# Kernel tuning notes

Measured on AMD Instinct MI355X. Metric: run time of the kernel, lower is better.

Reference implementation:

```python
import jax, jax.numpy as jnp
import numpy as np
import math

B, N, C, H = 8, 1024, 768, 12
D = C // H
HID = 4 * C
LS_INIT = 1e-6
LN_EPS = 1e-5


def setup_inputs() -> dict:
    key = jax.random.key(0)
    ks = jax.random.split(key, 8)
    s = lambda fan: 1.0 / math.sqrt(fan)
    return {
        'x': jax.random.normal(ks[0], (B, N, C), jnp.float32),
        'ln1_w': jnp.ones((C,), jnp.float32),
        'ln1_b': jnp.zeros((C,), jnp.float32),
        'qkv_w': jax.random.uniform(ks[1], (3 * C, C), jnp.float32, -s(C), s(C)),
        'qkv_b': jnp.zeros((3 * C,), jnp.float32),
        'proj_w': jax.random.uniform(ks[2], (C, C), jnp.float32, -s(C), s(C)),
        'proj_b': jnp.zeros((C,), jnp.float32),
        'attn_bias': jnp.asarray(-math.log(N), jnp.float32),
        'ls1': jnp.full((C,), LS_INIT, jnp.float32),
        'ln2_w': jnp.ones((C,), jnp.float32),
        'ln2_b': jnp.zeros((C,), jnp.float32),
        'w1': jax.random.uniform(ks[3], (HID, C), jnp.float32, -s(C), s(C)),
        'b1': jnp.zeros((HID,), jnp.float32),
        'w2': jax.random.uniform(ks[4], (C, HID), jnp.float32, -s(HID), s(HID)),
        'b2': jnp.zeros((C,), jnp.float32),
        'ls2': jnp.full((C,), LS_INIT, jnp.float32),
    }


def _layernorm(x, w, b):
    mu = jnp.mean(x, axis=-1, keepdims=True)
    var = jnp.mean(jnp.square(x - mu), axis=-1, keepdims=True)
    return (x - mu) * jax.lax.rsqrt(var + LN_EPS) * w + b


def reference(x, ln1_w, ln1_b, qkv_w, qkv_b, proj_w, proj_b, attn_bias,
              ls1, ln2_w, ln2_b, w1, b1, w2, b2, ls2):
    # --- sigmoid attention branch ---
    h = _layernorm(x, ln1_w, ln1_b)                       # [B,N,C]
    qkv = h @ qkv_w.T + qkv_b                              # [B,N,3C]
    qkv = qkv.reshape(B, N, 3, H, D).transpose(2, 0, 3, 1, 4)
    q, k, v = qkv[0], qkv[1], qkv[2]                       # [B,H,N,D]
    scale = D ** -0.5
    scores = jnp.einsum('bhnd,bhmd->bhnm', q, k) * scale + attn_bias
    attn = jax.nn.sigmoid(scores)                          # [B,H,N,N]
    o = jnp.einsum('bhnm,bhmd->bhnd', attn, v)             # [B,H,N,D]
    o = o.transpose(0, 2, 1, 3).reshape(B, N, C)
    o = o @ proj_w.T + proj_b
    x = x + o * ls1
    # --- MLP branch ---
    h2 = _layernorm(x, ln2_w, ln2_b)
    m = jax.nn.gelu(h2 @ w1.T + b1, approximate=False)
    m = m @ w2.T + b2
    x = x + m * ls2
    return x
```

## Files before the change

### kernel.cpp

```cpp
#include <hip/hip_runtime.h>
#include <math.h>

static constexpr int Bv   = 8;
static constexpr int Nv   = 1024;
static constexpr int Cv   = 768;
static constexpr int Hv   = 12;
static constexpr int HIDv = 3072;
static constexpr int Mv   = Bv * Nv;

typedef __attribute__((ext_vector_type(4)))  float f32x4;
typedef __attribute__((ext_vector_type(16))) float f32x16;
typedef __attribute__((ext_vector_type(8)))  short s16x8;
typedef __attribute__((ext_vector_type(4)))  short s16x4;

__device__ __forceinline__ short f2bf(float f) {
  union { float f; unsigned u; } c; c.f = f;
  unsigned r = c.u + 0x7fffu + ((c.u >> 16) & 1u);
  return (short)(r >> 16);
}

__device__ __forceinline__ void gload16(const void* g, void* l) {
  __builtin_amdgcn_global_load_lds(
      (const __attribute__((address_space(1))) unsigned*)g,
      (__attribute__((address_space(3))) unsigned*)l, 16, 0, 0);
}

__device__ __forceinline__ unsigned ldsaddr(const void* p) {
  return (unsigned)(size_t)(const __attribute__((address_space(3))) char*)p;
}

__device__ __forceinline__ float fsigmoid_exp2(float t) {
  return __builtin_amdgcn_rcpf(1.0f + __builtin_amdgcn_exp2f(t));
}

__global__ __launch_bounds__(256) void cvt4_kernel(const float* __restrict__ w0,
                                                   const float* __restrict__ w1,
                                                   const float* __restrict__ w2,
                                                   const float* __restrict__ w3,
                                                   short* __restrict__ o0,
                                                   short* __restrict__ o1,
                                                   short* __restrict__ o2,
                                                   short* __restrict__ o3) {
  int bid = blockIdx.x;
  const float* in; short* out; int i;
  if (bid < 1728)      { in = w0; out = o0; i = bid * 256 + threadIdx.x; }
  else if (bid < 2304) { in = w1; out = o1; i = (bid - 1728) * 256 + threadIdx.x; }
  else if (bid < 4608) { in = w2; out = o2; i = (bid - 2304) * 256 + threadIdx.x; }
  else                 { in = w3; out = o3; i = (bid - 4608) * 256 + threadIdx.x; }
  float4 v = ((const float4*)in)[i];
  short4 o;
  o.x = f2bf(v.x); o.y = f2bf(v.y); o.z = f2bf(v.z); o.w = f2bf(v.w);
  ((short4*)out)[i] = o;
}

__global__ __launch_bounds__(256) void ln_kernel(const float* __restrict__ x,
                                                 const float* __restrict__ w,
                                                 const float* __restrict__ b,
                                                 short* __restrict__ out) {
  const int wv = threadIdx.x >> 6, l = threadIdx.x & 63;
  const int row = blockIdx.x * 4 + wv;
  const float4* xr = (const float4*)(x + (size_t)row * Cv);
  float4 v[3];
  float s = 0.f, s2 = 0.f;
#pragma unroll
  for (int c = 0; c < 3; ++c) {
    v[c] = xr[c * 64 + l];
    s  += v[c].x + v[c].y + v[c].z + v[c].w;
    s2 += v[c].x * v[c].x + v[c].y * v[c].y + v[c].z * v[c].z + v[c].w * v[c].w;
  }
#pragma unroll
  for (int o = 32; o; o >>= 1) { s += __shfl_xor(s, o); s2 += __shfl_xor(s2, o); }
  const float mu  = s * (1.f / Cv);
  const float var = s2 * (1.f / Cv) - mu * mu;
  const float rs  = rsqrtf(var + 1e-5f);
  short4* orow = (short4*)(out + (size_t)row * Cv);
  const float4* wp = (const float4*)w;
  const float4* bp = (const float4*)b;
#pragma unroll
  for (int c = 0; c < 3; ++c) {
    float4 wv4 = wp[c * 64 + l], bv4 = bp[c * 64 + l];
    short4 o4;
    o4.x = f2bf((v[c].x - mu) * rs * wv4.x + bv4.x);
    o4.y = f2bf((v[c].y - mu) * rs * wv4.y + bv4.y);
    o4.z = f2bf((v[c].z - mu) * rs * wv4.z + bv4.z);
    o4.w = f2bf((v[c].w - mu) * rs * wv4.w + bv4.w);
    orow[c * 64 + l] = o4;
  }
}

template <int EPI>
__global__ __launch_bounds__(256) void gemm_bt(const short* __restrict__ A,
                                               const short* __restrict__ Bw,
                                               int Nn, int K,
                                               const float* __restrict__ bias,
                                               short* __restrict__ outB) {
  __shared__ __align__(16) short ldsA[2][128 * 32];
  __shared__ __align__(16) short ldsB[2][128 * 32];
  const int tid = threadIdx.x, w = tid >> 6, l = tid & 63;
  const int nbx = Nn >> 7;
  const int cpx = (int)gridDim.x >> 3;
  const int wg = ((int)blockIdx.x & 7) * cpx + ((int)blockIdx.x >> 3);
  const int bx = wg % nbx, by = wg / nbx;
  const int rowBase = by << 7, colBase = bx << 7;
  const int nK = K >> 5;
  const int wr = w >> 1, wc = w & 1;
  const int lrow = l >> 2, lcb = (l & 3) * 8;

  f32x4 acc[4][4] = {};

  auto stage = [&](int buf, int kt) {
    const short* abase = A  + (size_t)rowBase * K + kt * 32;
    const short* bbase = Bw + (size_t)colBase * K + kt * 32;
#pragma unroll
    for (int i = 0; i < 2; ++i) {
      int r = w * 2 + i;
      gload16(abase + (size_t)(r * 16 + lrow) * K + lcb, &ldsA[buf][r * 512]);
      gload16(bbase + (size_t)(r * 16 + lrow) * K + lcb, &ldsB[buf][r * 512]);
    }
  };

  stage(0, 0);
  __syncthreads();
  int cur = 0;
  for (int kt = 0; kt < nK; ++kt) {
    if (kt + 1 < nK) stage(cur ^ 1, kt + 1);
    s16x8 af[4], bfr[4];
#pragma unroll
    for (int i = 0; i < 4; ++i) {
      af[i]  = *(const s16x8*)&ldsA[cur][(wr * 64 + i * 16 + (l & 15)) * 32 + (l >> 4) * 8];
      bfr[i] = *(const s16x8*)&ldsB[cur][(wc * 64 + i * 16 + (l & 15)) * 32 + (l >> 4) * 8];
    }
#pragma unroll
    for (int i = 0; i < 4; ++i)
#pragma unroll
      for (int j = 0; j < 4; ++j)
        acc[i][j] = __builtin_amdgcn_mfma_f32_16x16x32_bf16(af[i], bfr[j], acc[i][j], 0, 0, 0);
    __syncthreads();
    cur ^= 1;
  }

#pragma unroll
  for (int i = 0; i < 4; ++i)
#pragma unroll
    for (int j = 0; j < 4; ++j) {
      const int col = colBase + wc * 64 + j * 16 + (l & 15);
      const float bcol = bias[col];
#pragma unroll
      for (int r4 = 0; r4 < 4; ++r4) {
        const int row = rowBase + wr * 64 + i * 16 + (l >> 4) * 4 + r4;
        float v = acc[i][j][r4] + bcol;
        if (EPI == 2) v = v * fsigmoid_exp2(v * -2.4554669f);
        outB[(size_t)row * Nn + col] = f2bf(v);
      }
    }
}

template <int EPI>
__global__ __launch_bounds__(256) void gemm_sm(const short* __restrict__ A,
                                               const short* __restrict__ Bw,
                                               int Nn, int K,
                                               const float* __restrict__ bias,
                                               const float* __restrict__ ls,
                                               const float* __restrict__ resid,
                                               float* __restrict__ outF) {
  __shared__ __align__(16) short ldsA[2][64 * 32];
  __shared__ __align__(16) short ldsB[2][128 * 32];
  const int tid = threadIdx.x, w = tid >> 6, l = tid & 63;
  const int nbx = Nn >> 7;
  const int cpx = (int)gridDim.x >> 3;
  const int wg = ((int)blockIdx.x & 7) * cpx + ((int)blockIdx.x >> 3);
  const int bx = wg % nbx, by = wg / nbx;
  const int rowBase = by << 6, colBase = bx << 7;
  const int nK = K >> 5;
  const int wr = w >> 1, wc = w & 1;
  const int lrow = l >> 2, lcb = (l & 3) * 8;

  f32x4 acc[2][4] = {};

  auto stage = [&](int buf, int kt) {
    const short* abase = A  + (size_t)rowBase * K + kt * 32;
    const short* bbase = Bw + (size_t)colBase * K + kt * 32;
    gload16(abase + (size_t)(w * 16 + lrow) * K + lcb, &ldsA[buf][w * 512]);
#pragma unroll
    for (int i = 0; i < 2; ++i) {
      int r = w * 2 + i;
      gload16(bbase + (size_t)(r * 16 + lrow) * K + lcb, &ldsB[buf][r * 512]);
    }
  };

  stage(0, 0);
  __syncthreads();
  int cur = 0;
  for (int kt = 0; kt < nK; ++kt) {
    if (kt + 1 < nK) stage(cur ^ 1, kt + 1);
    s16x8 af[2], bfr[4];
#pragma unroll
    for (int i = 0; i < 2; ++i)
      af[i]  = *(const s16x8*)&ldsA[cur][(wr * 32 + i * 16 + (l & 15)) * 32 + (l >> 4) * 8];
#pragma unroll
    for (int j = 0; j < 4; ++j)
      bfr[j] = *(const s16x8*)&ldsB[cur][(wc * 64 + j * 16 + (l & 15)) * 32 + (l >> 4) * 8];
#pragma unroll
    for (int i = 0; i < 2; ++i)
#pragma unroll
      for (int j = 0; j < 4; ++j)
        acc[i][j] = __builtin_amdgcn_mfma_f32_16x16x32_bf16(af[i], bfr[j], acc[i][j], 0, 0, 0);
    __syncthreads();
    cur ^= 1;
  }

#pragma unroll
  for (int i = 0; i < 2; ++i)
#pragma unroll
    for (int j = 0; j < 4; ++j) {
      const int col = colBase + wc * 64 + j * 16 + (l & 15);
      const float bcol = bias[col], lscol = ls[col];
#pragma unroll
      for (int r4 = 0; r4 < 4; ++r4) {
        const int row = rowBase + wr * 32 + i * 16 + (l >> 4) * 4 + r4;
        float v = (acc[i][j][r4] + bcol) * lscol;
        if (EPI == 1) {
          outF[(size_t)row * Nn + col] = v + resid[(size_t)row * Nn + col];
        } else {
          outF[(size_t)row * Nn + col] += v;
        }
      }
    }
}

__global__ __launch_bounds__(256) void attn_kernel(const short* __restrict__ qkv,
                                                   const float* __restrict__ pbias,
                                                   short* __restrict__ o) {
  __shared__ __align__(16) short ldsK[2][64 * 64];
  __shared__ __align__(16) short ldsV[2][64 * 64];
  const int tid = threadIdx.x, w = tid >> 6, l = tid & 63;
  const int qt = blockIdx.x & 7, bh = blockIdx.x >> 3;
  const int b = bh / Hv, h = bh % Hv;
  const int q0 = qt * 128;
  const float c1 = -0.125f * 1.44269504f;
  const float c0 = -pbias[0] * 1.44269504f;
  const size_t rstr = 3 * Cv;
  const short* qb = qkv + (size_t)b * Nv * rstr + h * 64;
  const short* kb = qb + Cv;
  const short* vb = qb + 2 * Cv;

  s16x8 qf[4];
  {
    const short* qrow = qb + (size_t)(q0 + w * 32 + (l & 31)) * rstr + (l >> 5) * 8;
#pragma unroll
    for (int dc = 0; dc < 4; ++dc) qf[dc] = *(const s16x8*)(qrow + dc * 16);
  }

  auto stage = [&](int buf, int t) {
#pragma unroll
    for (int i = 0; i < 2; ++i) {
      int r = w * 2 + i;
      int kv = r * 8 + (l >> 3);
      gload16(kb + (size_t)(t * 64 + kv) * rstr + (((l & 7) ^ (kv & 7)) << 3),
              &ldsK[buf][r * 512]);
      int s   = r * 8 + (l >> 3);
      int kv2 = ((s >> 2) << 2) + ((l & 7) >> 1);
      int d2  = ((s & 3) << 4) + ((l & 1) << 3);
      gload16(vb + (size_t)(t * 64 + kv2) * rstr + d2, &ldsV[buf][r * 512]);
    }
  };

  stage(0, 0);
  __syncthreads();

  f32x16 oacc[2] = {};
  int cur = 0;
  for (int t = 0; t < 16; ++t) {
    if (t + 1 < 16) stage(cur ^ 1, t + 1);

    f32x16 sacc[2] = {};
#pragma unroll
    for (int kvh = 0; kvh < 2; ++kvh) {
      const int kv = kvh * 32 + (l & 31);
#pragma unroll
      for (int dc = 0; dc < 4; ++dc) {
        s16x8 kf = *(const s16x8*)&ldsK[cur][kv * 64 + (((dc * 2 + (l >> 5)) ^ (kv & 7)) << 3)];
        sacc[kvh] = __builtin_amdgcn_mfma_f32_32x32x16_bf16(kf, qf[dc], sacc[kvh], 0, 0, 0);
      }
    }

    unsigned pw[4][4];
#pragma unroll
    for (int kvh = 0; kvh < 2; ++kvh) {
      float p[16];
#pragma unroll
      for (int r = 0; r < 16; ++r)
        p[r] = fsigmoid_exp2(sacc[kvh][r] * c1 + c0);
#pragma unroll
      for (int half = 0; half < 2; ++half) {
        const int c = kvh * 2 + half, rb = half * 8;
        unsigned a, bq, cc, dq;
        asm("v_cvt_pk_bf16_f32 %0,%1,%2" : "=v"(a)  : "v"(p[rb + 0]), "v"(p[rb + 1]));
        asm("v_cvt_pk_bf16_f32 %0,%1,%2" : "=v"(bq) : "v"(p[rb + 4]), "v"(p[rb + 5]));
        asm("v_cvt_pk_bf16_f32 %0,%1,%2" : "=v"(cc) : "v"(p[rb + 2]), "v"(p[rb + 3]));
        asm("v_cvt_pk_bf16_f32 %0,%1,%2" : "=v"(dq) : "v"(p[rb + 6]), "v"(p[rb + 7]));
        asm("v_permlane32_swap_b32 %0,%1" : "+v"(a),  "+v"(bq));
        asm("v_permlane32_swap_b32 %0,%1" : "+v"(cc), "+v"(dq));
        pw[c][0] = a; pw[c][1] = cc; pw[c][2] = bq; pw[c][3] = dq;
      }
    }

    const unsigned vlds = ldsaddr(&ldsV[cur][0]);
#pragma unroll
    for (int dt = 0; dt < 2; ++dt) {
      s16x4 t1[4], t2[4];
#pragma unroll
      for (int c = 0; c < 4; ++c) {
        int s1 = c * 16 + ((l >> 5) << 3) + dt * 2 + ((l >> 4) & 1);
        unsigned ad = vlds + (unsigned)(s1 * 128 + (l & 15) * 8);
        asm volatile("ds_read_b64_tr_b16 %0, %1"            : "=v"(t1[c]) : "v"(ad));
        asm volatile("ds_read_b64_tr_b16 %0, %1 offset:512" : "=v"(t2[c]) : "v"(ad));
      }
      asm volatile("s_waitcnt lgkmcnt(0)" ::: "memory");
      __builtin_amdgcn_sched_barrier(0);
#pragma unroll
      for (int c = 0; c < 4; ++c) {
        union { s16x4 q[2]; s16x8 v; } va;
        va.q[0] = t1[c]; va.q[1] = t2[c];
        union { unsigned u[4]; s16x8 v; } pb;
        pb.u[0] = pw[c][0]; pb.u[1] = pw[c][1]; pb.u[2] = pw[c][2]; pb.u[3] = pw[c][3];
        oacc[dt] = __builtin_amdgcn_mfma_f32_32x32x16_bf16(va.v, pb.v, oacc[dt], 0, 0, 0);
      }
    }

    __syncthreads();
    cur ^= 1;
  }

  __syncthreads();
  short* obuf = (short*)ldsK + w * 2048;
  {
    const int q = l & 31, hs = (l >> 5) << 3;
#pragma unroll
    for (int dt = 0; dt < 2; ++dt)
#pragma unroll
      for (int rg = 0; rg < 4; ++rg) {
        unsigned w0, w1;
        asm("v_cvt_pk_bf16_f32 %0,%1,%2" : "=v"(w0) : "v"(oacc[dt][rg * 4 + 0]), "v"(oacc[dt][rg * 4 + 1]));
        asm("v_cvt_pk_bf16_f32 %0,%1,%2" : "=v"(w1) : "v"(oacc[dt][rg * 4 + 2]), "v"(oacc[dt][rg * 4 + 3]));
        int slot = (dt * 4 + rg) ^ (q & 7);
        *(unsigned long long*)((char*)obuf + q * 128 + slot * 16 + hs) =
            (unsigned long long)w0 | ((unsigned long long)w1 << 32);
      }
  }
  __syncthreads();
  {
    const int q = l >> 1;
    const short* rrow = obuf + q * 64;
    short* orow = o + (size_t)(b * Nv + q0 + w * 32 + q) * Cv + h * 64 + (l & 1) * 32;
#pragma unroll
    for (int i = 0; i < 4; ++i) {
      int slot = (l & 1) * 4 + i;
      s16x8 vv = *(const s16x8*)(rrow + ((slot ^ (q & 7)) << 3));
      *(s16x8*)(orow + i * 8) = vv;
    }
  }
}

extern "C" void kernel_launch(void* const* d_in, const int* in_sizes, int n_in,
                              void* d_out, int out_size, void* d_ws, size_t ws_size,
                              hipStream_t stream) {
  const float* x      = (const float*)d_in[0];
  const float* ln1_w  = (const float*)d_in[1];
  const float* ln1_b  = (const float*)d_in[2];
  const float* qkv_w  = (const float*)d_in[3];
  const float* qkv_b  = (const float*)d_in[4];
  const float* proj_w = (const float*)d_in[5];
  const float* proj_b = (const float*)d_in[6];
  const float* attn_b = (const float*)d_in[7];
  const float* ls1    = (const float*)d_in[8];
  const float* ln2_w  = (const float*)d_in[9];
  const float* ln2_b  = (const float*)d_in[10];
  const float* w1     = (const float*)d_in[11];
  const float* b1     = (const float*)d_in[12];
  const float* w2     = (const float*)d_in[13];
  const float* b2     = (const float*)d_in[14];
  const float* ls2    = (const float*)d_in[15];
  float* out = (float*)d_out;

  char* ws = (char*)d_ws;
  short* wqkvb = (short*)ws;  ws += (size_t)3 * Cv * Cv * 2;
  short* wprjb = (short*)ws;  ws += (size_t)Cv * Cv * 2;
  short* w1b   = (short*)ws;  ws += (size_t)HIDv * Cv * 2;
  short* w2b   = (short*)ws;  ws += (size_t)Cv * HIDv * 2;
  short* bufA  = (short*)ws;  ws += (size_t)Mv * Cv * 2;
  short* bufB  = (short*)ws;

  cvt4_kernel<<<6912, 256, 0, stream>>>(qkv_w, proj_w, w1, w2,
                                        wqkvb, wprjb, w1b, w2b);

  ln_kernel<<<Mv / 4, 256, 0, stream>>>(x, ln1_w, ln1_b, bufA);
  gemm_bt<0><<<(Mv / 128) * (3 * Cv / 128), 256, 0, stream>>>(
      bufA, wqkvb, 3 * Cv, Cv, qkv_b, bufB);
  attn_kernel<<<Bv * Hv * (Nv / 128), 256, 0, stream>>>(bufB, attn_b, bufA);
  gemm_sm<1><<<(Mv / 64) * (Cv / 128), 256, 0, stream>>>(
      bufA, wprjb, Cv, Cv, proj_b, ls1, x, out);
  ln_kernel<<<Mv / 4, 256, 0, stream>>>(out, ln2_w, ln2_b, bufA);
  gemm_bt<2><<<(Mv / 128) * (HIDv / 128), 256, 0, stream>>>(
      bufA, w1b, HIDv, Cv, b1, bufB);
  gemm_sm<3><<<(Mv / 64) * (Cv / 128), 256, 0, stream>>>(
      bufB, w2b, Cv, HIDv, b2, ls2, nullptr, out);
}
```

Before: 375.9 us.

## Use split-K atomic GEMM for MLP down-projection and reorder LDS staging layout

The final MLP down-projection (K=3072) moves from 64x128 tiles to 128x128 tiles with a 2-way split-K, and each partial sum is accumulated into the output with float atomicAdd. The first split also adds the scaled bias. This is meant to raise per-block data reuse while keeping enough blocks to fill the GPU. Separately, all GEMMs change how global loads are mapped to LDS: each 16-row group now stores its four k-chunks contiguously, which alters both global access coalescing and LDS read bank patterns. The atomics add read-modify-write traffic on the output and make the floating-point summation order nondeterministic.

```diff
diff --git a/kernel.cpp b/kernel.cpp
--- a/kernel.cpp
+++ b/kernel.cpp
@@ -88,6 +88,7 @@
   }
 }
 
+
 template <int EPI>
 __global__ __launch_bounds__(256) void gemm_bt(const short* __restrict__ A,
                                                const short* __restrict__ Bw,
@@ -104,31 +105,32 @@
   const int rowBase = by << 7, colBase = bx << 7;
   const int nK = K >> 5;
   const int wr = w >> 1, wc = w & 1;
-  const int lrow = l >> 2, lcb = (l & 3) * 8;
+  const int srow = l & 15, skp = l >> 4;
 
   f32x4 acc[4][4] = {};
 
   auto stage = [&](int buf, int kt) {
-    const short* abase = A  + (size_t)rowBase * K + kt * 32;
-    const short* bbase = Bw + (size_t)colBase * K + kt * 32;
+    const short* abase = A  + (size_t)rowBase * K + kt * 32 + skp * 8;
+    const short* bbase = Bw + (size_t)colBase * K + kt * 32 + skp * 8;
 #pragma unroll
     for (int i = 0; i < 2; ++i) {
       int r = w * 2 + i;
-      gload16(abase + (size_t)(r * 16 + lrow) * K + lcb, &ldsA[buf][r * 512]);
-      gload16(bbase + (size_t)(r * 16 + lrow) * K + lcb, &ldsB[buf][r * 512]);
+      gload16(abase + (size_t)(r * 16 + srow) * K, &ldsA[buf][r * 512]);
+      gload16(bbase + (size_t)(r * 16 + srow) * K, &ldsB[buf][r * 512]);
     }
   };
 
   stage(0, 0);
   __syncthreads();
   int cur = 0;
+  const int fro = skp * 128 + srow * 8;
   for (int kt = 0; kt < nK; ++kt) {
     if (kt + 1 < nK) stage(cur ^ 1, kt + 1);
     s16x8 af[4], bfr[4];
 #pragma unroll
     for (int i = 0; i < 4; ++i) {
-      af[i]  = *(const s16x8*)&ldsA[cur][(wr * 64 + i * 16 + (l & 15)) * 32 + (l >> 4) * 8];
-      bfr[i] = *(const s16x8*)&ldsB[cur][(wc * 64 + i * 16 + (l & 15)) * 32 + (l >> 4) * 8];
+      af[i]  = *(const s16x8*)&ldsA[cur][(wr * 4 + i) * 512 + fro];
+      bfr[i] = *(const s16x8*)&ldsB[cur][(wc * 4 + i) * 512 + fro];
     }
 #pragma unroll
     for (int i = 0; i < 4; ++i)
@@ -155,7 +157,77 @@
     }
 }
 
-template <int EPI>
+__global__ __launch_bounds__(256) void gemm_atomic(const short* __restrict__ A,
+                                                   const short* __restrict__ Bw,
+                                                   int Nn, int K, int nks,
+                                                   const float* __restrict__ bias,
+                                                   const float* __restrict__ ls,
+                                                   float* __restrict__ outF) {
+  __shared__ __align__(16) short ldsA[2][128 * 32];
+  __shared__ __align__(16) short ldsB[2][128 * 32];
+  const int tid = threadIdx.x, w = tid >> 6, l = tid & 63;
+  const int nbx = Nn >> 7;
+  const int cpx = (int)gridDim.x >> 3;
+  const int wg = ((int)blockIdx.x & 7) * cpx + ((int)blockIdx.x >> 3);
+  const int per = (int)gridDim.x / nks;
+  const int ks = wg / per, rem = wg % per;
+  const int bx = rem % nbx, by = rem / nbx;
+  const int rowBase = by << 7, colBase = bx << 7;
+  const int kseg = K / nks;
+  const int k0 = ks * kseg;
+  const int nK = kseg >> 5;
+  const int wr = w >> 1, wc = w & 1;
+  const int srow = l & 15, skp = l >> 4;
+
+  f32x4 acc[4][4] = {};
+
+  auto stage = [&](int buf, int kt) {
+    const short* abase = A  + (size_t)rowBase * K + k0 + kt * 32 + skp * 8;
+    const short* bbase = Bw + (size_t)colBase * K + k0 + kt * 32 + skp * 8;
+#pragma unroll
+    for (int i = 0; i < 2; ++i) {
+      int r = w * 2 + i;
+      gload16(abase + (size_t)(r * 16 + srow) * K, &ldsA[buf][r * 512]);
+      gload16(bbase + (size_t)(r * 16 + srow) * K, &ldsB[buf][r * 512]);
+    }
+  };
+
+  stage(0, 0);
+  __syncthreads();
+  int cur = 0;
+  const int fro = skp * 128 + srow * 8;
+  for (int kt = 0; kt < nK; ++kt) {
+    if (kt + 1 < nK) stage(cur ^ 1, kt + 1);
+    s16x8 af[4], bfr[4];
+#pragma unroll
+    for (int i = 0; i < 4; ++i) {
+      af[i]  = *(const s16x8*)&ldsA[cur][(wr * 4 + i) * 512 + fro];
+      bfr[i] = *(const s16x8*)&ldsB[cur][(wc * 4 + i) * 512 + fro];
+    }
+#pragma unroll
+    for (int i = 0; i < 4; ++i)
+#pragma unroll
+      for (int j = 0; j < 4; ++j)
+        acc[i][j] = __builtin_amdgcn_mfma_f32_16x16x32_bf16(af[i], bfr[j], acc[i][j], 0, 0, 0);
+    __syncthreads();
+    cur ^= 1;
+  }
+
+#pragma unroll
+  for (int i = 0; i < 4; ++i)
+#pragma unroll
+    for (int j = 0; j < 4; ++j) {
+      const int col = colBase + wc * 64 + j * 16 + (l & 15);
+      const float lscol = ls[col];
+      const float addb = (ks == 0) ? bias[col] * lscol : 0.f;
+#pragma unroll
+      for (int r4 = 0; r4 < 4; ++r4) {
+        const int row = rowBase + wr * 64 + i * 16 + (l >> 4) * 4 + r4;
+        atomicAdd(&outF[(size_t)row * Nn + col], acc[i][j][r4] * lscol + addb);
+      }
+    }
+}
+
 __global__ __launch_bounds__(256) void gemm_sm(const short* __restrict__ A,
                                                const short* __restrict__ Bw,
                                                int Nn, int K,
@@ -173,33 +245,34 @@
   const int rowBase = by << 6, colBase = bx << 7;
   const int nK = K >> 5;
   const int wr = w >> 1, wc = w & 1;
-  const int lrow = l >> 2, lcb = (l & 3) * 8;
+  const int srow = l & 15, skp = l >> 4;
 
   f32x4 acc[2][4] = {};
 
   auto stage = [&](int buf, int kt) {
-    const short* abase = A  + (size_t)rowBase * K + kt * 32;
-    const short* bbase = Bw + (size_t)colBase * K + kt * 32;
-    gload16(abase + (size_t)(w * 16 + lrow) * K + lcb, &ldsA[buf][w * 512]);
+    const short* abase = A  + (size_t)rowBase * K + kt * 32 + skp * 8;
+    const short* bbase = Bw + (size_t)colBase * K + kt * 32 + skp * 8;
+    gload16(abase + (size_t)(w * 16 + srow) * K, &ldsA[buf][w * 512]);
 #pragma unroll
     for (int i = 0; i < 2; ++i) {
       int r = w * 2 + i;
-      gload16(bbase + (size_t)(r * 16 + lrow) * K + lcb, &ldsB[buf][r * 512]);
+      gload16(bbase + (size_t)(r * 16 + srow) * K, &ldsB[buf][r * 512]);
     }
   };
 
   stage(0, 0);
   __syncthreads();
   int cur = 0;
+  const int fro = skp * 128 + srow * 8;
   for (int kt = 0; kt < nK; ++kt) {
     if (kt + 1 < nK) stage(cur ^ 1, kt + 1);
     s16x8 af[2], bfr[4];
 #pragma unroll
     for (int i = 0; i < 2; ++i)
-      af[i]  = *(const s16x8*)&ldsA[cur][(wr * 32 + i * 16 + (l & 15)) * 32 + (l >> 4) * 8];
+      af[i]  = *(const s16x8*)&ldsA[cur][(wr * 2 + i) * 512 + fro];
 #pragma unroll
     for (int j = 0; j < 4; ++j)
-      bfr[j] = *(const s16x8*)&ldsB[cur][(wc * 64 + j * 16 + (l & 15)) * 32 + (l >> 4) * 8];
+      bfr[j] = *(const s16x8*)&ldsB[cur][(wc * 4 + j) * 512 + fro];
 #pragma unroll
     for (int i = 0; i < 2; ++i)
 #pragma unroll
@@ -219,11 +292,7 @@
       for (int r4 = 0; r4 < 4; ++r4) {
         const int row = rowBase + wr * 32 + i * 16 + (l >> 4) * 4 + r4;
         float v = (acc[i][j][r4] + bcol) * lscol;
-        if (EPI == 1) {
-          outF[(size_t)row * Nn + col] = v + resid[(size_t)row * Nn + col];
-        } else {
-          outF[(size_t)row * Nn + col] += v;
-        }
+        outF[(size_t)row * Nn + col] = v + resid[(size_t)row * Nn + col];
       }
     }
 }
@@ -398,11 +467,11 @@
   gemm_bt<0><<<(Mv / 128) * (3 * Cv / 128), 256, 0, stream>>>(
       bufA, wqkvb, 3 * Cv, Cv, qkv_b, bufB);
   attn_kernel<<<Bv * Hv * (Nv / 128), 256, 0, stream>>>(bufB, attn_b, bufA);
-  gemm_sm<1><<<(Mv / 64) * (Cv / 128), 256, 0, stream>>>(
+  gemm_sm<<<(Mv / 64) * (Cv / 128), 256, 0, stream>>>(
       bufA, wprjb, Cv, Cv, proj_b, ls1, x, out);
   ln_kernel<<<Mv / 4, 256, 0, stream>>>(out, ln2_w, ln2_b, bufA);
   gemm_bt<2><<<(Mv / 128) * (HIDv / 128), 256, 0, stream>>>(
       bufA, w1b, HIDv, Cv, b1, bufB);
-  gemm_sm<3><<<(Mv / 64) * (Cv / 128), 256, 0, stream>>>(
-      bufB, w2b, Cv, HIDv, b2, ls2, nullptr, out);
-}
+  gemm_atomic<<<(Mv / 128) * (Cv / 128) * 2, 256, 0, stream>>>(
+      bufB, w2b, Cv, HIDv, 2, b2, ls2, out);
+}
```

Result: slower. 454.5 us (+20.9%).
